# Kernel tuning notes

Measured on AMD Instinct MI355X. Metric: run time of the kernel, lower is better.

## Reference

```python
import jax, jax.numpy as jnp
import numpy as np

N, E, D, H, C, L = 50000, 600000, 128, 128, 40, 2
NEG_SLOPE = 0.1


def setup_inputs() -> dict:
    key = jax.random.key(0)
    ks = jax.random.split(key, 12)

    def lin(k, din, dout):
        return (jax.random.normal(k, (din, dout), jnp.float32) / np.sqrt(din)).astype(jnp.float32)

    x = jax.random.normal(ks[0], (N, D), jnp.float32)
    edge_index = jax.random.randint(ks[1], (2, E), 0, N, dtype=jnp.int32)
    return {
        "x": x,
        "edge_index": edge_index,
        "enc_Wl": lin(ks[2], D, H),
        "enc_Wr": lin(ks[3], D, H),
        "enc_b": jnp.zeros((H,), jnp.float32),
        "lay_Wl": jnp.stack([lin(jax.random.fold_in(ks[4], i), H, H) for i in range(L)]),
        "lay_Wr": jnp.stack([lin(jax.random.fold_in(ks[5], i), H, H) for i in range(L)]),
        "lay_b": jnp.zeros((L, H), jnp.float32),
        "dec_Wl": lin(ks[6], H, C),
        "dec_Wr": lin(ks[7], H, C),
        "dec_b": jnp.zeros((C,), jnp.float32),
    }


def _sage(x, src, dst, inv_cnt, Wl, Wr, b):
    # mean-aggregate neighbor messages: gather x[src], scatter-sum to dst, divide by degree
    agg = jax.ops.segment_sum(x[src], dst, num_segments=N) * inv_cnt  # [N, d_in]
    return agg @ Wl + x @ Wr + b


def reference(x, edge_index, enc_Wl, enc_Wr, enc_b, lay_Wl, lay_Wr, lay_b, dec_Wl, dec_Wr, dec_b):
    src, dst = edge_index[0], edge_index[1]
    # in-degree per target node, clamped to 1 (PyG scatter-mean semantics: isolated nodes get 0)
    deg = jax.ops.segment_sum(jnp.ones((E,), jnp.float32), dst, num_segments=N)
    inv_cnt = (1.0 / jnp.maximum(deg, 1.0))[:, None]  # [N, 1]

    h = jax.nn.leaky_relu(_sage(x, src, dst, inv_cnt, enc_Wl, enc_Wr, enc_b), NEG_SLOPE)
    for i in range(L):
        h = jax.nn.leaky_relu(_sage(h, src, dst, inv_cnt, lay_Wl[i], lay_Wr[i], lay_b[i]), NEG_SLOPE)
    out = _sage(h, src, dst, inv_cnt, dec_Wl, dec_Wr, dec_b)
    return jax.nn.log_softmax(out, axis=1)
```

## Files before the change

### kernel.cpp

```cpp
#include <hip/hip_runtime.h>
#include <hip/hip_bf16.h>

#define NN 50000
#define EE 600000
#define HH 128
#define CC 40
#define NEG 0.1f
#define SCAN_NB 196

typedef __attribute__((ext_vector_type(8))) short bf16x8;
typedef __attribute__((ext_vector_type(4))) float f32x4;

__device__ __forceinline__ unsigned short f2bf(float f) {
    unsigned u = __float_as_uint(f);
    unsigned r = u + 0x7fffu + ((u >> 16) & 1u);
    return (unsigned short)(r >> 16);
}
__device__ __forceinline__ float bfhi(unsigned v) { return __uint_as_float(v & 0xFFFF0000u); }
__device__ __forceinline__ float bflo(unsigned v) { return __uint_as_float(v << 16); }


__global__ void k_count(const int* __restrict__ dst, int* __restrict__ counts) {
    int t = blockIdx.x * blockDim.x + threadIdx.x;
    if (t < EE / 4) {
        int4 d = ((const int4*)dst)[t];
        if ((unsigned)d.x < (unsigned)NN) atomicAdd(&counts[d.x], 1);
        if ((unsigned)d.y < (unsigned)NN) atomicAdd(&counts[d.y], 1);
        if ((unsigned)d.z < (unsigned)NN) atomicAdd(&counts[d.z], 1);
        if ((unsigned)d.w < (unsigned)NN) atomicAdd(&counts[d.w], 1);
    }
}

__global__ void k_scanA(const int* __restrict__ counts, int* __restrict__ blocksums) {
    int t = threadIdx.x, b = blockIdx.x;
    int i = b * 256 + t;
    int v = (i < NN) ? counts[i] : 0;
    for (int off = 1; off < 64; off <<= 1) v += __shfl_xor(v, off, 64);
    __shared__ int ws[4];
    if ((t & 63) == 0) ws[t >> 6] = v;
    __syncthreads();
    if (t == 0) blocksums[b] = ws[0] + ws[1] + ws[2] + ws[3];
}

__global__ void k_scanC(const int* __restrict__ counts, const int* __restrict__ blocksums,
                        int* __restrict__ offsets, int* __restrict__ cursor,
                        float* __restrict__ inv) {
    int t = threadIdx.x, b = blockIdx.x, lane = t & 63, w = t >> 6;
    __shared__ int ws1[4];
    __shared__ int ws2[4];
    int r = (t < SCAN_NB && t < b) ? blocksums[t] : 0;
    for (int off = 1; off < 64; off <<= 1) r += __shfl_xor(r, off, 64);
    if (lane == 0) ws1[w] = r;
    __syncthreads();
    int blockoff = ws1[0] + ws1[1] + ws1[2] + ws1[3];
    int i = b * 256 + t;
    int c = (i < NN) ? counts[i] : 0;
    int v = c;
    for (int off = 1; off < 64; off <<= 1) {
        int u = __shfl_up(v, off, 64);
        if (lane >= off) v += u;
    }
    if (lane == 63) ws2[w] = v;
    __syncthreads();
    int woff = 0;
    for (int j = 0; j < w; ++j) woff += ws2[j];
    int excl = blockoff + woff + (v - c);
    if (i < NN) {
        offsets[i] = excl;
        cursor[i]  = excl;
        inv[i] = (c > 0) ? 1.0f / (float)c : 1.0f;
    }
    if (b == SCAN_NB - 1 && t == 0) offsets[NN] = blockoff + blocksums[SCAN_NB - 1];
}

__global__ void k_scatter(const int* __restrict__ src, const int* __restrict__ dst,
                          int* __restrict__ cursor, int* __restrict__ csr) {
    int t = blockIdx.x * blockDim.x + threadIdx.x;
    if (t < EE / 4) {
        int4 s = ((const int4*)src)[t];
        int4 d = ((const int4*)dst)[t];
        if ((unsigned)d.x < (unsigned)NN) csr[atomicAdd(&cursor[d.x], 1)] = s.x;
        if ((unsigned)d.y < (unsigned)NN) csr[atomicAdd(&cursor[d.y], 1)] = s.y;
        if ((unsigned)d.z < (unsigned)NN) csr[atomicAdd(&cursor[d.z], 1)] = s.z;
        if ((unsigned)d.w < (unsigned)NN) csr[atomicAdd(&cursor[d.w], 1)] = s.w;
    }
}

struct SwzArgs {
    const float* src[8];
    unsigned short* dst[8];
};

template <int DOUT, int DOUTP>
__device__ __forceinline__ void swz_one(const float* __restrict__ W,
                                        unsigned short* __restrict__ dstf, int idx) {
    int k = idx / DOUTP, n = idx % DOUTP;
    unsigned short val = (n < DOUT) ? f2bf(W[k * DOUT + n]) : (unsigned short)0;
    int kt = k >> 5, kin = k & 31, nt = n >> 4, nin = n & 15;
    int lane = ((kin >> 3) << 4) | nin;
    int j = kin & 7;
    int NT = DOUTP >> 4;
    dstf[(((kt * NT + nt) * 64) + lane) * 8 + j] = val;
}

__global__ void k_swz_all(SwzArgs a) {
    int b = blockIdx.x;
    if (b < 384) {
        int which = b >> 6;
        int idx = (b & 63) * 256 + threadIdx.x;
        swz_one<HH, HH>(a.src[which], a.dst[which], idx);
    } else {
        int bb = b - 384;
        int which = 6 + bb / 24;
        int idx = (bb % 24) * 256 + threadIdx.x;
        swz_one<CC, 48>(a.src[which], a.dst[which], idx);
    }
}

template <int NT, int MODE, int INF32>
__global__ __launch_bounds__(256) void k_fused(
    const void* __restrict__ hin_v,
    const int* __restrict__ offsets, const int* __restrict__ csr,
    const float* __restrict__ inv,
    const unsigned short* __restrict__ B1f, const unsigned short* __restrict__ B2f,
    const float* __restrict__ bias, void* __restrict__ out_v) {
    __shared__ unsigned lds[16][72];
    int wid = threadIdx.x >> 6;
    int lane = threadIdx.x & 63;
    int m0 = blockIdx.x * 16;

    int beg[4], end[4];
    int maxd = 0;
#pragma unroll
    for (int n = 0; n < 4; ++n) {
        int node = m0 + wid * 4 + n;
        beg[n] = offsets[node];
        end[n] = offsets[node + 1];
        int d = end[n] - beg[n];
        maxd = maxd > d ? maxd : d;
    }

    if (INF32) {
        const float4* hf4 = (const float4*)hin_v;
        int g = lane & 31, s = lane >> 5;
        float acc[4][4];
#pragma unroll
        for (int n = 0; n < 4; ++n)
#pragma unroll
            for (int d = 0; d < 4; ++d) acc[n][d] = 0.f;
        int rounds = (maxd + 1) >> 1;

        float4 v[4]; int ok[4];
        auto issue = [&](int r, float4* vv, int* okk) {
#pragma unroll
            for (int n = 0; n < 4; ++n) {
                int idx = beg[n] + r * 2 + s;
                int o = idx < end[n];
                int row = csr[o ? idx : 0];
                vv[n] = hf4[(size_t)row * 32 + g];
                okk[n] = o;
            }
        };
        if (rounds > 0) {
            issue(0, v, ok);
            for (int r = 0; r < rounds; ++r) {
                float4 vn[4]; int okn[4];
                bool more = (r + 1 < rounds);
                if (more) issue(r + 1, vn, okn);
#pragma unroll
                for (int n = 0; n < 4; ++n) {
                    if (ok[n]) {
                        acc[n][0] += v[n].x; acc[n][1] += v[n].y;
                        acc[n][2] += v[n].z; acc[n][3] += v[n].w;
                    }
                }
                if (more) {
#pragma unroll
                    for (int n = 0; n < 4; ++n) { v[n] = vn[n]; ok[n] = okn[n]; }
                }
            }
        }
#pragma unroll
        for (int n = 0; n < 4; ++n) {
#pragma unroll
            for (int d = 0; d < 4; ++d) {
                float t = acc[n][d];
                t += __shfl_xor(t, 32, 64);
                acc[n][d] = t;
            }
            float sc = inv[m0 + wid * 4 + n];
            if (s == 0) {
                unsigned d0 = ((unsigned)f2bf(acc[n][1] * sc) << 16) | f2bf(acc[n][0] * sc);
                unsigned d1 = ((unsigned)f2bf(acc[n][3] * sc) << 16) | f2bf(acc[n][2] * sc);
                uint2 w2; w2.x = d0; w2.y = d1;
                *(uint2*)&lds[wid * 4 + n][2 * g] = w2;
            }
        }
    } else {
        const uint4* hw4 = (const uint4*)hin_v;
        int g = lane & 15, s = lane >> 4;
        float acc[4][8];
#pragma unroll
        for (int n = 0; n < 4; ++n)
#pragma unroll
            for (int d = 0; d < 8; ++d) acc[n][d] = 0.f;
        int rounds = (maxd + 3) >> 2;

        uint4 v[4]; int ok[4];
        auto issue = [&](int r, uint4* vv, int* okk) {
#pragma unroll
            for (int n = 0; n < 4; ++n) {
                int idx = beg[n] + r * 4 + s;
                int o = idx < end[n];
                int row = csr[o ? idx : 0];
                vv[n] = hw4[(size_t)row * 16 + g];
                okk[n] = o;
            }
        };
        if (rounds > 0) {
            issue(0, v, ok);
            for (int r = 0; r < rounds; ++r) {
                uint4 vn[4]; int okn[4];
                bool more = (r + 1 < rounds);
                if (more) issue(r + 1, vn, okn);
#pragma unroll
                for (int n = 0; n < 4; ++n) {
                    if (ok[n]) {
                        acc[n][0] += bflo(v[n].x); acc[n][1] += bfhi(v[n].x);
                        acc[n][2] += bflo(v[n].y); acc[n][3] += bfhi(v[n].y);
                        acc[n][4] += bflo(v[n].z); acc[n][5] += bfhi(v[n].z);
                        acc[n][6] += bflo(v[n].w); acc[n][7] += bfhi(v[n].w);
                    }
                }
                if (more) {
#pragma unroll
                    for (int n = 0; n < 4; ++n) { v[n] = vn[n]; ok[n] = okn[n]; }
                }
            }
        }
#pragma unroll
        for (int n = 0; n < 4; ++n) {
#pragma unroll
            for (int d = 0; d < 8; ++d) {
                float t = acc[n][d];
                t += __shfl_xor(t, 16, 64);
                t += __shfl_xor(t, 32, 64);
                acc[n][d] = t;
            }
            float sc = inv[m0 + wid * 4 + n];
            if (s == 0) {
                uint4 w4;
                w4.x = ((unsigned)f2bf(acc[n][1] * sc) << 16) | f2bf(acc[n][0] * sc);
                w4.y = ((unsigned)f2bf(acc[n][3] * sc) << 16) | f2bf(acc[n][2] * sc);
                w4.z = ((unsigned)f2bf(acc[n][5] * sc) << 16) | f2bf(acc[n][4] * sc);
                w4.w = ((unsigned)f2bf(acc[n][7] * sc) << 16) | f2bf(acc[n][6] * sc);
                *(uint4*)&lds[wid * 4 + n][4 * g] = w4;
            }
        }
    }
    __syncthreads();

    if (MODE == 1 && wid != 0) return;

    int nin = lane & 15;
    int kq = lane >> 4;
    const unsigned* arow = &lds[nin][0];
    constexpr int TW = (MODE == 0) ? 2 : NT;

    f32x4 acc[TW];
#pragma unroll
    for (int j = 0; j < TW; ++j) acc[j] = (f32x4){0.f, 0.f, 0.f, 0.f};

#pragma unroll
    for (int kt = 0; kt < 4; ++kt) {
        bf16x8 a1 = *(const bf16x8*)(arow + kt * 16 + kq * 4);
        bf16x8 a2;
        if (INF32) {
            const float* hf = (const float*)hin_v;
            const float* rp = hf + (m0 + nin) * HH + kt * 32 + kq * 8;
            float4 p0 = *(const float4*)(rp);
            float4 p1 = *(const float4*)(rp + 4);
            a2[0] = (short)f2bf(p0.x); a2[1] = (short)f2bf(p0.y);
            a2[2] = (short)f2bf(p0.z); a2[3] = (short)f2bf(p0.w);
            a2[4] = (short)f2bf(p1.x); a2[5] = (short)f2bf(p1.y);
            a2[6] = (short)f2bf(p1.z); a2[7] = (short)f2bf(p1.w);
        } else {
            const unsigned short* hb = (const unsigned short*)hin_v;
            a2 = *(const bf16x8*)(hb + (m0 + nin) * HH + kt * 32 + kq * 8);
        }
#pragma unroll
        for (int j = 0; j < TW; ++j) {
            int tile = (MODE == 0) ? (wid * 2 + j) : j;
            bf16x8 b1 = *(const bf16x8*)(B1f + (((kt * NT + tile) * 64) + lane) * 8);
            acc[j] = __builtin_amdgcn_mfma_f32_16x16x32_bf16(a1, b1, acc[j], 0, 0, 0);
        }
#pragma unroll
        for (int j = 0; j < TW; ++j) {
            int tile = (MODE == 0) ? (wid * 2 + j) : j;
            bf16x8 b2 = *(const bf16x8*)(B2f + (((kt * NT + tile) * 64) + lane) * 8);
            acc[j] = __builtin_amdgcn_mfma_f32_16x16x32_bf16(a2, b2, acc[j], 0, 0, 0);
        }
    }

    if (MODE == 0) {
        unsigned short* out = (unsigned short*)out_v;
#pragma unroll
        for (int j = 0; j < TW; ++j) {
            int col = (wid * 2 + j) * 16 + nin;
            float bv = bias[col];
#pragma unroll
            for (int r = 0; r < 4; ++r) {
                int m = m0 + kq * 4 + r;
                float v = acc[j][r] + bv;
                v = fmaxf(v, NEG * v);
                out[m * HH + col] = f2bf(v);
            }
        }
    } else {
        float* out = (float*)out_v;
        float bv[NT];
#pragma unroll
        for (int t = 0; t < NT; ++t) {
            int col = t * 16 + nin;
            bv[t] = (col < CC) ? bias[col] : 0.f;
        }
#pragma unroll
        for (int r = 0; r < 4; ++r) {
            int m = m0 + kq * 4 + r;
            float v[NT];
            float mx = -1e30f;
#pragma unroll
            for (int t = 0; t < NT; ++t) {
                int col = t * 16 + nin;
                v[t] = acc[t][r] + bv[t];
                if (col < CC) mx = fmaxf(mx, v[t]);
            }
            for (int off = 1; off < 16; off <<= 1) mx = fmaxf(mx, __shfl_xor(mx, off, 64));
            float sm = 0.f;
#pragma unroll
            for (int t = 0; t < NT; ++t) {
                int col = t * 16 + nin;
                if (col < CC) sm += expf(v[t] - mx);
            }
            for (int off = 1; off < 16; off <<= 1) sm += __shfl_xor(sm, off, 64);
            float lse = mx + logf(sm);
#pragma unroll
            for (int t = 0; t < NT; ++t) {
                int col = t * 16 + nin;
                if (col < CC) out[m * CC + col] = v[t] - lse;
            }
        }
    }
}

extern "C" void kernel_launch(void* const* d_in, const int* in_sizes, int n_in,
                              void* d_out, int out_size, void* d_ws, size_t ws_size,
                              hipStream_t stream) {
    const float* x      = (const float*)d_in[0];
    const int*   ei     = (const int*)d_in[1];
    const float* enc_Wl = (const float*)d_in[2];
    const float* enc_Wr = (const float*)d_in[3];
    const float* enc_b  = (const float*)d_in[4];
    const float* lay_Wl = (const float*)d_in[5];
    const float* lay_Wr = (const float*)d_in[6];
    const float* lay_b  = (const float*)d_in[7];
    const float* dec_Wl = (const float*)d_in[8];
    const float* dec_Wr = (const float*)d_in[9];
    const float* dec_b  = (const float*)d_in[10];
    float* out = (float*)d_out;

    const int* src = ei;
    const int* dst = ei + EE;

    char* p = (char*)d_ws;
    auto carve = [&](size_t bytes) {
        char* r = p;
        p += (bytes + 255) & ~(size_t)255;
        return r;
    };
    int*            counts    = (int*)carve(NN * 4);
    int*            offsets   = (int*)carve((NN + 1) * 4);
    int*            cursor    = (int*)carve(NN * 4);
    int*            csr       = (int*)carve(EE * 4);
    float*          inv       = (float*)carve(NN * 4);
    int*            blocksums = (int*)carve(SCAN_NB * 4);
    unsigned short* h1        = (unsigned short*)carve((size_t)NN * HH * 2);
    unsigned short* h2        = (unsigned short*)carve((size_t)NN * HH * 2);
    unsigned short* wf[8];
    for (int i = 0; i < 6; ++i) wf[i] = (unsigned short*)carve(HH * HH * 2);
    wf[6] = (unsigned short*)carve(HH * 48 * 2);
    wf[7] = (unsigned short*)carve(HH * 48 * 2);

    {
        SwzArgs a;
        a.src[0] = enc_Wl; a.src[1] = enc_Wr;
        a.src[2] = lay_Wl; a.src[3] = lay_Wr;
        a.src[4] = lay_Wl + HH * HH; a.src[5] = lay_Wr + HH * HH;
        a.src[6] = dec_Wl; a.src[7] = dec_Wr;
        for (int i = 0; i < 8; ++i) a.dst[i] = wf[i];
        k_swz_all<<<432, 256, 0, stream>>>(a);
    }

    hipMemsetAsync(counts, 0, NN * 4, stream);
    int eblk4 = (EE / 4 + 255) / 256;
    k_count<<<eblk4, 256, 0, stream>>>(dst, counts);
    k_scanA<<<SCAN_NB, 256, 0, stream>>>(counts, blocksums);
    k_scanC<<<SCAN_NB, 256, 0, stream>>>(counts, blocksums, offsets, cursor, inv);
    k_scatter<<<eblk4, 256, 0, stream>>>(src, dst, cursor, csr);

    const int FB = NN / 16;
    k_fused<8, 0, 1><<<FB, 256, 0, stream>>>(x,  offsets, csr, inv, wf[0], wf[1], enc_b,      h1);
    k_fused<8, 0, 0><<<FB, 256, 0, stream>>>(h1, offsets, csr, inv, wf[2], wf[3], lay_b,      h2);
    k_fused<8, 0, 0><<<FB, 256, 0, stream>>>(h2, offsets, csr, inv, wf[4], wf[5], lay_b + HH, h1);
    k_fused<3, 1, 0><<<FB, 256, 0, stream>>>(h1, offsets, csr, inv, wf[6], wf[7], dec_b,      out);
}
```

Measured before the change: 339.5 us.

## Project decoder features before aggregation and cast input to bf16 upfront

Casts x to bf16 in a separate kernel so the encoder uses the same bf16 gather path. Restructures the layer gather into four feature phases, with 16 neighbours gathered in parallel per wave. For the decoder it first computes h·Wl at width 48 in a pre-pass and then aggregates those narrower rows, using the linearity of mean aggregation to cut gather bytes. This adds extra kernel launches and a bf16 rounding of the projected values before aggregation.

```diff
diff --git a/kernel.cpp b/kernel.cpp
--- a/kernel.cpp
+++ b/kernel.cpp
@@ -86,6 +86,17 @@
     }
 }
 
+__global__ void k_xcast(const float* __restrict__ x, unsigned* __restrict__ xb) {
+    int t = blockIdx.x * 256 + threadIdx.x;
+    if (t < NN * HH / 4) {
+        float4 v = ((const float4*)x)[t];
+        uint2 o;
+        o.x = ((unsigned)f2bf(v.y) << 16) | f2bf(v.x);
+        o.y = ((unsigned)f2bf(v.w) << 16) | f2bf(v.z);
+        ((uint2*)xb)[t] = o;
+    }
+}
+
 struct SwzArgs {
     const float* src[8];
     unsigned short* dst[8];
@@ -117,103 +128,49 @@
     }
 }
 
-template <int NT, int MODE, int INF32>
-__global__ __launch_bounds__(256) void k_fused(
-    const void* __restrict__ hin_v,
+__global__ __launch_bounds__(256) void k_layer(
+    const unsigned short* __restrict__ hin,
     const int* __restrict__ offsets, const int* __restrict__ csr,
     const float* __restrict__ inv,
     const unsigned short* __restrict__ B1f, const unsigned short* __restrict__ B2f,
-    const float* __restrict__ bias, void* __restrict__ out_v) {
+    const float* __restrict__ bias, unsigned short* __restrict__ out) {
     __shared__ unsigned lds[16][72];
     int wid = threadIdx.x >> 6;
     int lane = threadIdx.x & 63;
     int m0 = blockIdx.x * 16;
+    int g = lane & 3;
+    int s = lane >> 2;
+    const uint4* hw4 = (const uint4*)hin;
 
     int beg[4], end[4];
+    float sc[4];
     int maxd = 0;
 #pragma unroll
     for (int n = 0; n < 4; ++n) {
         int node = m0 + wid * 4 + n;
         beg[n] = offsets[node];
         end[n] = offsets[node + 1];
+        sc[n] = inv[node];
         int d = end[n] - beg[n];
         maxd = maxd > d ? maxd : d;
     }
-
-    if (INF32) {
-        const float4* hf4 = (const float4*)hin_v;
-        int g = lane & 31, s = lane >> 5;
-        float acc[4][4];
+    int rounds = (maxd + 15) >> 4;
+
+    for (int ph = 0; ph < 4; ++ph) {
+        float acc[4][8];
 #pragma unroll
         for (int n = 0; n < 4; ++n)
 #pragma unroll
-            for (int d = 0; d < 4; ++d) acc[n][d] = 0.f;
-        int rounds = (maxd + 1) >> 1;
-
-        float4 v[4]; int ok[4];
-        auto issue = [&](int r, float4* vv, int* okk) {
+            for (int d = 0; d < 8; ++d) acc[n][d] = 0.f;
+
+        uint4 v[4]; int ok[4];
+        auto issue = [&](int r, uint4* vv, int* okk) {
 #pragma unroll
             for (int n = 0; n < 4; ++n) {
-                int idx = beg[n] + r * 2 + s;
+                int idx = beg[n] + r * 16 + s;
                 int o = idx < end[n];
                 int row = csr[o ? idx : 0];
-                vv[n] = hf4[(size_t)row * 32 + g];
-                okk[n] = o;
-            }
-        };
-        if (rounds > 0) {
-            issue(0, v, ok);
-            for (int r = 0; r < rounds; ++r) {
-                float4 vn[4]; int okn[4];
-                bool more = (r + 1 < rounds);
-                if (more) issue(r + 1, vn, okn);
-#pragma unroll
-                for (int n = 0; n < 4; ++n) {
-                    if (ok[n]) {
-                        acc[n][0] += v[n].x; acc[n][1] += v[n].y;
-                        acc[n][2] += v[n].z; acc[n][3] += v[n].w;
-                    }
-                }
-                if (more) {
-#pragma unroll
-                    for (int n = 0; n < 4; ++n) { v[n] = vn[n]; ok[n] = okn[n]; }
-                }
-            }
-        }
-#pragma unroll
-        for (int n = 0; n < 4; ++n) {
-#pragma unroll
-            for (int d = 0; d < 4; ++d) {
-                float t = acc[n][d];
-                t += __shfl_xor(t, 32, 64);
-                acc[n][d] = t;
-            }
-            float sc = inv[m0 + wid * 4 + n];
-            if (s == 0) {
-                unsigned d0 = ((unsigned)f2bf(acc[n][1] * sc) << 16) | f2bf(acc[n][0] * sc);
-                unsigned d1 = ((unsigned)f2bf(acc[n][3] * sc) << 16) | f2bf(acc[n][2] * sc);
-                uint2 w2; w2.x = d0; w2.y = d1;
-                *(uint2*)&lds[wid * 4 + n][2 * g] = w2;
-            }
-        }
-    } else {
-        const uint4* hw4 = (const uint4*)hin_v;
-        int g = lane & 15, s = lane >> 4;
-        float acc[4][8];
-#pragma unroll
-        for (int n = 0; n < 4; ++n)
-#pragma unroll
-            for (int d = 0; d < 8; ++d) acc[n][d] = 0.f;
-        int rounds = (maxd + 3) >> 2;
-
-        uint4 v[4]; int ok[4];
-        auto issue = [&](int r, uint4* vv, int* okk) {
-#pragma unroll
-            for (int n = 0; n < 4; ++n) {
-                int idx = beg[n] + r * 4 + s;
-                int o = idx < end[n];
-                int row = csr[o ? idx : 0];
-                vv[n] = hw4[(size_t)row * 16 + g];
+                vv[n] = hw4[(size_t)row * 16 + ph * 4 + g];
                 okk[n] = o;
             }
         };
@@ -243,112 +200,232 @@
 #pragma unroll
             for (int d = 0; d < 8; ++d) {
                 float t = acc[n][d];
+                t += __shfl_xor(t, 4, 64);
+                t += __shfl_xor(t, 8, 64);
                 t += __shfl_xor(t, 16, 64);
                 t += __shfl_xor(t, 32, 64);
                 acc[n][d] = t;
             }
-            float sc = inv[m0 + wid * 4 + n];
             if (s == 0) {
                 uint4 w4;
-                w4.x = ((unsigned)f2bf(acc[n][1] * sc) << 16) | f2bf(acc[n][0] * sc);
-                w4.y = ((unsigned)f2bf(acc[n][3] * sc) << 16) | f2bf(acc[n][2] * sc);
-                w4.z = ((unsigned)f2bf(acc[n][5] * sc) << 16) | f2bf(acc[n][4] * sc);
-                w4.w = ((unsigned)f2bf(acc[n][7] * sc) << 16) | f2bf(acc[n][6] * sc);
-                *(uint4*)&lds[wid * 4 + n][4 * g] = w4;
+                w4.x = ((unsigned)f2bf(acc[n][1] * sc[n]) << 16) | f2bf(acc[n][0] * sc[n]);
+                w4.y = ((unsigned)f2bf(acc[n][3] * sc[n]) << 16) | f2bf(acc[n][2] * sc[n]);
+                w4.z = ((unsigned)f2bf(acc[n][5] * sc[n]) << 16) | f2bf(acc[n][4] * sc[n]);
+                w4.w = ((unsigned)f2bf(acc[n][7] * sc[n]) << 16) | f2bf(acc[n][6] * sc[n]);
+                *(uint4*)&lds[wid * 4 + n][ph * 16 + g * 4] = w4;
             }
         }
     }
     __syncthreads();
-
-    if (MODE == 1 && wid != 0) return;
 
     int nin = lane & 15;
     int kq = lane >> 4;
     const unsigned* arow = &lds[nin][0];
-    constexpr int TW = (MODE == 0) ? 2 : NT;
-
-    f32x4 acc[TW];
-#pragma unroll
-    for (int j = 0; j < TW; ++j) acc[j] = (f32x4){0.f, 0.f, 0.f, 0.f};
+
+    f32x4 acc[2];
+    acc[0] = (f32x4){0.f, 0.f, 0.f, 0.f};
+    acc[1] = (f32x4){0.f, 0.f, 0.f, 0.f};
 
 #pragma unroll
     for (int kt = 0; kt < 4; ++kt) {
         bf16x8 a1 = *(const bf16x8*)(arow + kt * 16 + kq * 4);
-        bf16x8 a2;
-        if (INF32) {
-            const float* hf = (const float*)hin_v;
-            const float* rp = hf + (m0 + nin) * HH + kt * 32 + kq * 8;
-            float4 p0 = *(const float4*)(rp);
-            float4 p1 = *(const float4*)(rp + 4);
-            a2[0] = (short)f2bf(p0.x); a2[1] = (short)f2bf(p0.y);
-            a2[2] = (short)f2bf(p0.z); a2[3] = (short)f2bf(p0.w);
-            a2[4] = (short)f2bf(p1.x); a2[5] = (short)f2bf(p1.y);
-            a2[6] = (short)f2bf(p1.z); a2[7] = (short)f2bf(p1.w);
-        } else {
-            const unsigned short* hb = (const unsigned short*)hin_v;
-            a2 = *(const bf16x8*)(hb + (m0 + nin) * HH + kt * 32 + kq * 8);
-        }
-#pragma unroll
-        for (int j = 0; j < TW; ++j) {
-            int tile = (MODE == 0) ? (wid * 2 + j) : j;
-            bf16x8 b1 = *(const bf16x8*)(B1f + (((kt * NT + tile) * 64) + lane) * 8);
+        bf16x8 a2 = *(const bf16x8*)(hin + (size_t)(m0 + nin) * HH + kt * 32 + kq * 8);
+#pragma unroll
+        for (int j = 0; j < 2; ++j) {
+            int tile = wid * 2 + j;
+            bf16x8 b1 = *(const bf16x8*)(B1f + (((kt * 8 + tile) * 64) + lane) * 8);
             acc[j] = __builtin_amdgcn_mfma_f32_16x16x32_bf16(a1, b1, acc[j], 0, 0, 0);
         }
 #pragma unroll
-        for (int j = 0; j < TW; ++j) {
-            int tile = (MODE == 0) ? (wid * 2 + j) : j;
-            bf16x8 b2 = *(const bf16x8*)(B2f + (((kt * NT + tile) * 64) + lane) * 8);
+        for (int j = 0; j < 2; ++j) {
+            int tile = wid * 2 + j;
+            bf16x8 b2 = *(const bf16x8*)(B2f + (((kt * 8 + tile) * 64) + lane) * 8);
             acc[j] = __builtin_amdgcn_mfma_f32_16x16x32_bf16(a2, b2, acc[j], 0, 0, 0);
         }
     }
 
-    if (MODE == 0) {
-        unsigned short* out = (unsigned short*)out_v;
-#pragma unroll
-        for (int j = 0; j < TW; ++j) {
-            int col = (wid * 2 + j) * 16 + nin;
-            float bv = bias[col];
-#pragma unroll
-            for (int r = 0; r < 4; ++r) {
-                int m = m0 + kq * 4 + r;
-                float v = acc[j][r] + bv;
-                v = fmaxf(v, NEG * v);
-                out[m * HH + col] = f2bf(v);
-            }
-        }
-    } else {
-        float* out = (float*)out_v;
-        float bv[NT];
-#pragma unroll
-        for (int t = 0; t < NT; ++t) {
-            int col = t * 16 + nin;
-            bv[t] = (col < CC) ? bias[col] : 0.f;
-        }
+#pragma unroll
+    for (int j = 0; j < 2; ++j) {
+        int col = (wid * 2 + j) * 16 + nin;
+        float bv = bias[col];
 #pragma unroll
         for (int r = 0; r < 4; ++r) {
             int m = m0 + kq * 4 + r;
-            float v[NT];
-            float mx = -1e30f;
-#pragma unroll
-            for (int t = 0; t < NT; ++t) {
-                int col = t * 16 + nin;
-                v[t] = acc[t][r] + bv[t];
-                if (col < CC) mx = fmaxf(mx, v[t]);
-            }
-            for (int off = 1; off < 16; off <<= 1) mx = fmaxf(mx, __shfl_xor(mx, off, 64));
-            float sm = 0.f;
-#pragma unroll
-            for (int t = 0; t < NT; ++t) {
-                int col = t * 16 + nin;
-                if (col < CC) sm += expf(v[t] - mx);
-            }
-            for (int off = 1; off < 16; off <<= 1) sm += __shfl_xor(sm, off, 64);
-            float lse = mx + logf(sm);
-#pragma unroll
-            for (int t = 0; t < NT; ++t) {
-                int col = t * 16 + nin;
-                if (col < CC) out[m * CC + col] = v[t] - lse;
-            }
+            float v = acc[j][r] + bv;
+            v = fmaxf(v, NEG * v);
+            out[(size_t)m * HH + col] = f2bf(v);
+        }
+    }
+}
+
+__global__ __launch_bounds__(256) void k_pre(const unsigned short* __restrict__ h1,
+                                             const unsigned short* __restrict__ Bf,
+                                             unsigned short* __restrict__ t) {
+    int wave = (blockIdx.x * 256 + threadIdx.x) >> 6;
+    int lane = threadIdx.x & 63;
+    int m0 = wave * 16;
+    if (m0 >= NN) return;
+    int nin = lane & 15, kq = lane >> 4;
+    f32x4 acc[3];
+#pragma unroll
+    for (int j = 0; j < 3; ++j) acc[j] = (f32x4){0.f, 0.f, 0.f, 0.f};
+#pragma unroll
+    for (int kt = 0; kt < 4; ++kt) {
+        bf16x8 a = *(const bf16x8*)(h1 + (size_t)(m0 + nin) * HH + kt * 32 + kq * 8);
+#pragma unroll
+        for (int j = 0; j < 3; ++j) {
+            bf16x8 b = *(const bf16x8*)(Bf + (((kt * 3 + j) * 64) + lane) * 8);
+            acc[j] = __builtin_amdgcn_mfma_f32_16x16x32_bf16(a, b, acc[j], 0, 0, 0);
+        }
+    }
+#pragma unroll
+    for (int j = 0; j < 3; ++j) {
+        int col = j * 16 + nin;
+#pragma unroll
+        for (int r = 0; r < 4; ++r) {
+            int m = m0 + kq * 4 + r;
+            t[(size_t)m * 64 + col] = f2bf(acc[j][r]);
+        }
+    }
+    int col2 = 48 + nin;
+#pragma unroll
+    for (int r = 0; r < 4; ++r) t[(size_t)(m0 + kq * 4 + r) * 64 + col2] = 0;
+}
+
+__global__ __launch_bounds__(256) void k_dec(
+    const unsigned short* __restrict__ tbuf,
+    const unsigned short* __restrict__ h1,
+    const int* __restrict__ offsets, const int* __restrict__ csr,
+    const float* __restrict__ inv,
+    const unsigned short* __restrict__ B2f, const float* __restrict__ bias,
+    float* __restrict__ out) {
+    __shared__ float aggT[16][52];
+    int wid = threadIdx.x >> 6;
+    int lane = threadIdx.x & 63;
+    int m0 = blockIdx.x * 16;
+    int g = lane & 7;
+    int s = lane >> 3;
+    const uint4* t4 = (const uint4*)tbuf;
+
+    int beg[4], end[4];
+    float sc[4];
+    int maxd = 0;
+#pragma unroll
+    for (int n = 0; n < 4; ++n) {
+        int node = m0 + wid * 4 + n;
+        beg[n] = offsets[node];
+        end[n] = offsets[node + 1];
+        sc[n] = inv[node];
+        int d = end[n] - beg[n];
+        maxd = maxd > d ? maxd : d;
+    }
+    int rounds = (maxd + 7) >> 3;
+
+    float acc[4][8];
+#pragma unroll
+    for (int n = 0; n < 4; ++n)
+#pragma unroll
+        for (int d = 0; d < 8; ++d) acc[n][d] = 0.f;
+
+    uint4 v[4]; int ok[4];
+    auto issue = [&](int r, uint4* vv, int* okk) {
+#pragma unroll
+        for (int n = 0; n < 4; ++n) {
+            int idx = beg[n] + r * 8 + s;
+            int o = idx < end[n];
+            int row = csr[o ? idx : 0];
+            vv[n] = t4[(size_t)row * 8 + g];
+            okk[n] = o;
+        }
+    };
+    if (rounds > 0) {
+        issue(0, v, ok);
+        for (int r = 0; r < rounds; ++r) {
+            uint4 vn[4]; int okn[4];
+            bool more = (r + 1 < rounds);
+            if (more) issue(r + 1, vn, okn);
+#pragma unroll
+            for (int n = 0; n < 4; ++n) {
+                if (ok[n]) {
+                    acc[n][0] += bflo(v[n].x); acc[n][1] += bfhi(v[n].x);
+                    acc[n][2] += bflo(v[n].y); acc[n][3] += bfhi(v[n].y);
+                    acc[n][4] += bflo(v[n].z); acc[n][5] += bfhi(v[n].z);
+                    acc[n][6] += bflo(v[n].w); acc[n][7] += bfhi(v[n].w);
+                }
+            }
+            if (more) {
+#pragma unroll
+                for (int n = 0; n < 4; ++n) { v[n] = vn[n]; ok[n] = okn[n]; }
+            }
+        }
+    }
+#pragma unroll
+    for (int n = 0; n < 4; ++n) {
+#pragma unroll
+        for (int d = 0; d < 8; ++d) {
+            float t = acc[n][d];
+            t += __shfl_xor(t, 8, 64);
+            t += __shfl_xor(t, 16, 64);
+            t += __shfl_xor(t, 32, 64);
+            acc[n][d] = t;
+        }
+        if (s == 0 && g < 6) {
+            float4 p0, p1;
+            p0.x = acc[n][0] * sc[n]; p0.y = acc[n][1] * sc[n];
+            p0.z = acc[n][2] * sc[n]; p0.w = acc[n][3] * sc[n];
+            p1.x = acc[n][4] * sc[n]; p1.y = acc[n][5] * sc[n];
+            p1.z = acc[n][6] * sc[n]; p1.w = acc[n][7] * sc[n];
+            *(float4*)&aggT[wid * 4 + n][8 * g] = p0;
+            *(float4*)&aggT[wid * 4 + n][8 * g + 4] = p1;
+        }
+    }
+    __syncthreads();
+    if (wid != 0) return;
+
+    int nin = lane & 15, kq = lane >> 4;
+    f32x4 acc2[3];
+#pragma unroll
+    for (int j = 0; j < 3; ++j) acc2[j] = (f32x4){0.f, 0.f, 0.f, 0.f};
+#pragma unroll
+    for (int kt = 0; kt < 4; ++kt) {
+        bf16x8 a2 = *(const bf16x8*)(h1 + (size_t)(m0 + nin) * HH + kt * 32 + kq * 8);
+#pragma unroll
+        for (int j = 0; j < 3; ++j) {
+            bf16x8 b2 = *(const bf16x8*)(B2f + (((kt * 3 + j) * 64) + lane) * 8);
+            acc2[j] = __builtin_amdgcn_mfma_f32_16x16x32_bf16(a2, b2, acc2[j], 0, 0, 0);
+        }
+    }
+    float bv[3];
+#pragma unroll
+    for (int t = 0; t < 3; ++t) {
+        int col = t * 16 + nin;
+        bv[t] = (col < CC) ? bias[col] : 0.f;
+    }
+#pragma unroll
+    for (int r = 0; r < 4; ++r) {
+        int m = m0 + kq * 4 + r;
+        int ml = kq * 4 + r;
+        float v[3];
+        float mx = -1e30f;
+#pragma unroll
+        for (int t = 0; t < 3; ++t) {
+            int col = t * 16 + nin;
+            v[t] = acc2[t][r] + aggT[ml][col] + bv[t];
+            if (col < CC) mx = fmaxf(mx, v[t]);
+        }
+        for (int off = 1; off < 16; off <<= 1) mx = fmaxf(mx, __shfl_xor(mx, off, 64));
+        float sm = 0.f;
+#pragma unroll
+        for (int t = 0; t < 3; ++t) {
+            int col = t * 16 + nin;
+            if (col < CC) sm += expf(v[t] - mx);
+        }
+        for (int off = 1; off < 16; off <<= 1) sm += __shfl_xor(sm, off, 64);
+        float lse = mx + logf(sm);
+#pragma unroll
+        for (int t = 0; t < 3; ++t) {
+            int col = t * 16 + nin;
+            if (col < CC) out[(size_t)m * CC + col] = v[t] - lse;
         }
     }
 }
@@ -408,9 +485,13 @@
     k_scanC<<<SCAN_NB, 256, 0, stream>>>(counts, blocksums, offsets, cursor, inv);
     k_scatter<<<eblk4, 256, 0, stream>>>(src, dst, cursor, csr);
 
+    k_xcast<<<(NN * HH / 4 + 255) / 256, 256, 0, stream>>>(x, (unsigned*)h2);
+
     const int FB = NN / 16;
-    k_fused<8, 0, 1><<<FB, 256, 0, stream>>>(x,  offsets, csr, inv, wf[0], wf[1], enc_b,      h1);
-    k_fused<8, 0, 0><<<FB, 256, 0, stream>>>(h1, offsets, csr, inv, wf[2], wf[3], lay_b,      h2);
-    k_fused<8, 0, 0><<<FB, 256, 0, stream>>>(h2, offsets, csr, inv, wf[4], wf[5], lay_b + HH, h1);
-    k_fused<3, 1, 0><<<FB, 256, 0, stream>>>(h1, offsets, csr, inv, wf[6], wf[7], dec_b,      out);
-}
+    k_layer<<<FB, 256, 0, stream>>>(h2, offsets, csr, inv, wf[0], wf[1], enc_b,      h1);
+    k_layer<<<FB, 256, 0, stream>>>(h1, offsets, csr, inv, wf[2], wf[3], lay_b,      h2);
+    k_layer<<<FB, 256, 0, stream>>>(h2, offsets, csr, inv, wf[4], wf[5], lay_b + HH, h1);
+
+    k_pre<<<(NN / 16 + 3) / 4, 256, 0, stream>>>(h1, wf[6], h2);
+    k_dec<<<FB, 256, 0, stream>>>(h2, h1, offsets, csr, inv, wf[7], dec_b, out);
+}
```

After: 442.7 us. 30.4% more time.
